# Kernel optimization log

Measured on AMD Instinct MI355X. Metric: run time of the kernel, lower is better.

Reference implementation:

```python
import jax, jax.numpy as jnp
import numpy as np

HEADS, DIM_HEADS = 16, 16
SCALE = DIM_HEADS ** -0.5

# (forward_perm, inverse_perm) for each axial dim of x: (B, S, E, H, W)
# axial axes are 1 (seq), 3 (H=4), 4 (W=5); emb axis 2 moved to last, axial axis to second-last
_PERMS = [
    ((0, 3, 4, 1, 2), (0, 3, 4, 1, 2)),  # seq axis (self-inverse)
    ((0, 1, 4, 3, 2), (0, 1, 4, 3, 2)),  # H axis (self-inverse)
    ((0, 1, 3, 4, 2), (0, 1, 4, 2, 3)),  # W axis
]


def _self_attn(x, wq, wkv, wo_w, wo_b):
    # x: (..., t, d); standard multi-head self-attention along t
    q = x @ wq.T                               # (..., t, 256)
    k, v = jnp.split(x @ wkv.T, 2, axis=-1)    # each (..., t, 256)
    lead, tlen = x.shape[:-2], x.shape[-2]
    sh = (*lead, tlen, HEADS, DIM_HEADS)
    q, k, v = q.reshape(sh), k.reshape(sh), v.reshape(sh)
    scores = jnp.einsum('...thd,...shd->...hts', q, k) * SCALE
    attn = jax.nn.softmax(scores, axis=-1)
    o = jnp.einsum('...hts,...shd->...thd', attn, v)
    o = o.reshape(*lead, tlen, HEADS * DIM_HEADS)
    return o @ wo_w.T + wo_b


def _axial_attention_layer(x, wq_l, wkv_l, wo_w_l, wo_b_l):
    # sum of attention along each axial dim (sum_axial_out=True)
    out = jnp.zeros_like(x)
    for a, (p, ip) in enumerate(_PERMS):
        y = jnp.transpose(x, p)
        y = _self_attn(y, wq_l[a], wkv_l[a], wo_w_l[a], wo_b_l[a])
        out = out + jnp.transpose(y, ip)
    return out


def setup_inputs() -> dict:
    key = jax.random.key(0)
    ks = jax.random.split(key, 8)
    B, S, E, H, W = 32, 64, 256, 4, 5
    return {
        'x': jax.random.normal(ks[0], (B, S, E, H, W), jnp.float32),
        'pos_s': jax.random.normal(ks[1], (1, S, E, 1, 1), jnp.float32),
        'pos_h': jax.random.normal(ks[2], (1, 1, E, H, 1), jnp.float32),
        'pos_w': jax.random.normal(ks[3], (1, 1, E, 1, W), jnp.float32),
        'wq': jax.random.normal(ks[4], (2, 3, 256, E), jnp.float32) * 0.02,
        'wkv': jax.random.normal(ks[5], (2, 3, 512, E), jnp.float32) * 0.02,
        'wo_w': jax.random.normal(ks[6], (2, 3, E, 256), jnp.float32) * 0.02,
        'wo_b': jnp.zeros((2, 3, E), jnp.float32),
        'dec_w': jax.random.normal(ks[7], (1, E), jnp.float32) * 0.02,
        'dec_b': jnp.zeros((1,), jnp.float32),
    }


def reference(x, pos_s, pos_h, pos_w, wq, wkv, wo_w, wo_b, dec_w, dec_b):
    # additive axial positional embeddings
    x = x + pos_s + pos_h + pos_w
    # two stacked AxialAttention blocks (no residual in the wrapper)
    for l in range(2):
        x = _axial_attention_layer(x, wq[l], wkv[l], wo_w[l], wo_b[l])
    # (B, S, E, H, W) -> (B, S, H, W, E), linear decode to 1 channel, sigmoid
    x = jnp.transpose(x, (0, 1, 3, 4, 2))
    return jax.nn.sigmoid(x @ dec_w.T + dec_b)
```

## Files before the change

kernel.cpp:

```cpp
#include <hip/hip_runtime.h>
#include <stdint.h>

typedef unsigned short u16;
typedef u16 u16x8 __attribute__((ext_vector_type(8)));
typedef __bf16 bf16x8 __attribute__((ext_vector_type(8)));
typedef float f32x4 __attribute__((ext_vector_type(4)));
typedef float f32x16 __attribute__((ext_vector_type(16)));

#define NE   256
#define NPOS 40960
#define QLD  1536

__device__ __forceinline__ float bf2f(u16 h) {
  union { unsigned u; float f; } c; c.u = ((unsigned)h) << 16; return c.f;
}
__device__ __forceinline__ u16 f2bf(float f) {
  union { float f; unsigned u; } c; c.f = f;
  unsigned u = c.u;
  return (u16)((u + 0x7FFFu + ((u >> 16) & 1u)) >> 16);
}
__device__ __forceinline__ unsigned pkbf(float a, float b) {
  unsigned r;
  asm("v_cvt_pk_bf16_f32 %0, %1, %2" : "=v"(r) : "v"(a), "v"(b));
  return r;
}
__device__ __forceinline__ void gll16(const void* g, void* l) {
  __builtin_amdgcn_global_load_lds(
      (const __attribute__((address_space(1))) void*)g,
      (__attribute__((address_space(3))) void*)l, 16, 0, 0);
}
template<int N> __device__ __forceinline__ void waitvm() {
  if constexpr (N == 0)       asm volatile("s_waitcnt vmcnt(0)"  ::: "memory");
  else if constexpr (N == 4)  asm volatile("s_waitcnt vmcnt(4)"  ::: "memory");
  else if constexpr (N == 6)  asm volatile("s_waitcnt vmcnt(6)"  ::: "memory");
  else if constexpr (N == 8)  asm volatile("s_waitcnt vmcnt(8)"  ::: "memory");
  else if constexpr (N == 12) asm volatile("s_waitcnt vmcnt(12)" ::: "memory");
}

__global__ __launch_bounds__(256) void prep_kernel(
    const float* __restrict__ x, const float* __restrict__ pos_s,
    const float* __restrict__ pos_h, const float* __restrict__ pos_w,
    u16* __restrict__ xb)
{
  __shared__ float Ls[256 * 21];
  const int bs = blockIdx.x;
  const int s  = bs & 63;
  const int tid = threadIdx.x;
  const float* xp = x + (size_t)bs * 5120;
  for (int i = tid; i < 5120; i += 256) {
    int e = i / 20, hw = i % 20;
    int h = hw / 5, w = hw % 5;
    float v = xp[i] + pos_s[s * 256 + e] + pos_h[e * 4 + h] + pos_w[e * 5 + w];
    Ls[e * 21 + hw] = v;
  }
  __syncthreads();
  u16* op = xb + (size_t)bs * 20 * 256;
  for (int i = tid; i < 5120; i += 256) {
    int nl = i >> 8, e = i & 255;
    op[nl * 256 + e] = f2bf(Ls[e * 21 + nl]);
  }
}

#define PK_T1 (6*768*256)
#define PK_T2 (2*256*768)
__global__ __launch_bounds__(256) void pack_all(
    const float* __restrict__ wq, const float* __restrict__ wkv,
    const float* __restrict__ wo, const float* __restrict__ wo_b,
    u16* __restrict__ wqp, u16* __restrict__ wop, float* __restrict__ bsum)
{
  int i = blockIdx.x * 256 + threadIdx.x;
  if (i < PK_T1) {
    int la = i / (768 * 256);
    int rem = i - la * (768 * 256);
    int r = rem >> 8, c = rem & 255;
    float v = (r < 256) ? wq[(size_t)la * 65536 + r * 256 + c] * 0.25f
                        : wkv[(size_t)la * 131072 + (r - 256) * 256 + c];
    wqp[i] = f2bf(v);
  } else if (i < PK_T1 + PK_T2) {
    int j = i - PK_T1;
    int l = j / 196608;
    int rem = j - l * 196608;
    int out = rem / 768, k = rem % 768;
    int a = k >> 8, in = k & 255;
    wop[j] = f2bf(wo[(size_t)(((l * 3 + a) * 256) + out) * 256 + in]);
  } else if (i < PK_T1 + PK_T2 + 512) {
    int j = i - PK_T1 - PK_T2;
    int l = j >> 8, c = j & 255;
    bsum[j] = wo_b[(l * 3 + 0) * 256 + c] + wo_b[(l * 3 + 1) * 256 + c]
            + wo_b[(l * 3 + 2) * 256 + c];
  }
}

template<int MODE, int NKT, int NBN>
__global__ __launch_bounds__(256, 2) void gemm_bt(
    const u16* __restrict__ A, const u16* __restrict__ B,
    u16* __restrict__ Cb, const float* __restrict__ bias,
    const float* __restrict__ dw, float* __restrict__ logit,
    int ldc)
{
  constexpr int K   = NKT * 32;
  constexpr int BN  = 128;
  constexpr int NF  = BN / 32;
  constexpr int LPT = 2 + BN / 64;
  constexpr int ASZ = 128 * 32;
  constexpr int TSZ = (128 + BN) * 32;
  static_assert(NKT >= 2, "");

  __shared__ alignas(16) u16 smem[3 * TSZ];

  const int bid = blockIdx.x;
  const int cpx = gridDim.x >> 3;
  const int mapped = (bid & 7) * cpx + (bid >> 3);
  const int bm = mapped / NBN, bn = mapped % NBN;

  const int tid  = threadIdx.x;
  const int lane = tid & 63, w = tid >> 6;
  const int wr   = (w >> 1) * 64, wc = (w & 1) * (BN / 2);
  const int r16  = lane & 15, khi = lane >> 4;

  f32x4 acc[4][NF] = {};

  const u16* gA = A + (size_t)bm * 128 * K;
  const u16* gB = B + (size_t)bn * BN * K;

  auto STAGE = [&](int kt, int which) {
    u16* As = smem + which * TSZ;
    u16* Bs = As + ASZ;
    const u16* tA = gA + kt * 32;
    const u16* tB = gB + kt * 32;
    #pragma unroll
    for (int r = 0; r < 2; ++r) {
      int i = tid + r * 256;
      int row = i >> 2, seg = (i & 3) << 3;
      gll16(tA + (size_t)row * K + seg, (char*)As + i * 16);
    }
    #pragma unroll
    for (int r = 0; r < BN / 64; ++r) {
      int i = tid + r * 256;
      int row = i >> 2, seg = (i & 3) << 3;
      gll16(tB + (size_t)row * K + seg, (char*)Bs + i * 16);
    }
  };

  STAGE(0, 0);
  STAGE(1, 1);
  #pragma unroll
  for (int kt = 0; kt < NKT; ++kt) {
    const int cur = kt % 3;
    if (kt + 2 < NKT)      { STAGE(kt + 2, (kt + 2) % 3); waitvm<2 * LPT>(); }
    else if (kt + 1 < NKT) { waitvm<LPT>(); }
    else                   { waitvm<0>(); }
    __builtin_amdgcn_s_barrier();
    asm volatile("" ::: "memory");

    const u16* As = smem + cur * TSZ;
    const u16* Bs = As + ASZ;
    bf16x8 af[4], bfr[NF];
    #pragma unroll
    for (int m = 0; m < 4; ++m)
      af[m] = *(const bf16x8*)(As + (wr + m * 16 + r16) * 32 + khi * 8);
    #pragma unroll
    for (int n = 0; n < NF; ++n)
      bfr[n] = *(const bf16x8*)(Bs + (wc + n * 16 + r16) * 32 + khi * 8);
    #pragma unroll
    for (int m = 0; m < 4; ++m)
      #pragma unroll
      for (int n = 0; n < NF; ++n)
        acc[m][n] = __builtin_amdgcn_mfma_f32_16x16x32_bf16(af[m], bfr[n], acc[m][n], 0, 0, 0);

    asm volatile("" ::: "memory");
    __builtin_amdgcn_s_barrier();
  }

  const int row0 = bm * 128 + wr + khi * 4;
  const int col0 = bn * BN + wc + r16;

  if constexpr (MODE == 4) {
    float dwv[NF], bvv[NF];
    #pragma unroll
    for (int n = 0; n < NF; ++n) {
      int c = col0 + n * 16;
      dwv[n] = dw[c];
      bvv[n] = bias[c];
    }
    #pragma unroll
    for (int m = 0; m < 4; ++m) {
      #pragma unroll
      for (int j = 0; j < 4; ++j) {
        float p = 0.f;
        #pragma unroll
        for (int n = 0; n < NF; ++n) p += (acc[m][n][j] + bvv[n]) * dwv[n];
        p += __shfl_xor(p, 1);
        p += __shfl_xor(p, 2);
        p += __shfl_xor(p, 4);
        p += __shfl_xor(p, 8);
        if (r16 == 0) atomicAdd(&logit[row0 + m * 16 + j], p);
      }
    }
  } else {
    #pragma unroll
    for (int m = 0; m < 4; ++m) {
      #pragma unroll
      for (int n = 0; n < NF; ++n) {
        int c = col0 + n * 16;
        float bv = (MODE == 3) ? bias[c] : 0.f;
        #pragma unroll
        for (int j = 0; j < 4; ++j) {
          int r = row0 + m * 16 + j;
          Cb[(size_t)r * ldc + c] = f2bf(acc[m][n][j] + bv);
        }
      }
    }
  }
}

__global__ __launch_bounds__(256) void attn_seq_mfma(
    const u16* __restrict__ QKV, u16* __restrict__ Ob)
{
  const int w = threadIdx.x >> 6, lane = threadIdx.x & 63;
  const int wid = blockIdx.x * 4 + w;
  const int hd = wid & 15, g = wid >> 4;
  const int gb = g / 20, gr = g % 20;
  const int nbase = gb * 1280 + gr;
  const int lo = lane & 31, hi = lane >> 5;

  bf16x8 kf[2], qf[2];
  #pragma unroll
  for (int t = 0; t < 2; ++t) {
    size_t r = (size_t)(nbase + (lo + 32 * t) * 20) * QLD;
    kf[t] = *(const bf16x8*)(QKV + r + 256 + hd * 16 + hi * 8);
    qf[t] = *(const bf16x8*)(QKV + r +       hd * 16 + hi * 8);
  }
  union { u16 a[8]; bf16x8 v; } vt[4];
  #pragma unroll
  for (int c = 0; c < 4; ++c)
    #pragma unroll
    for (int j = 0; j < 8; ++j)
      vt[c].a[j] = QKV[(size_t)(nbase + (c * 16 + hi * 8 + j) * 20) * QLD
                       + 512 + hd * 16 + lo];

  f32x16 s00 = {}, s10 = {}, s01 = {}, s11 = {};
  s00 = __builtin_amdgcn_mfma_f32_32x32x16_bf16(kf[0], qf[0], s00, 0, 0, 0);
  s10 = __builtin_amdgcn_mfma_f32_32x32x16_bf16(kf[1], qf[0], s10, 0, 0, 0);
  s01 = __builtin_amdgcn_mfma_f32_32x32x16_bf16(kf[0], qf[1], s01, 0, 0, 0);
  s11 = __builtin_amdgcn_mfma_f32_32x32x16_bf16(kf[1], qf[1], s11, 0, 0, 0);

  auto run_qt = [&](f32x16 t0, f32x16 t1, int qt) {
    float m = -1e30f;
    #pragma unroll
    for (int r = 0; r < 16; ++r) { m = fmaxf(m, t0[r]); m = fmaxf(m, t1[r]); }
    m = fmaxf(m, __shfl_xor(m, 32));
    const float C = 1.4426950408889634f;
    float mc = m * C;
    float sum = 0.f;
    #pragma unroll
    for (int r = 0; r < 16; ++r) {
      float p0 = __builtin_amdgcn_exp2f(t0[r] * C - mc);
      float p1 = __builtin_amdgcn_exp2f(t1[r] * C - mc);
      t0[r] = p0; t1[r] = p1; sum += p0; sum += p1;
    }
    sum += __shfl_xor(sum, 32);
    float inv = __builtin_amdgcn_rcpf(sum);
    #pragma unroll
    for (int r = 0; r < 16; ++r) { t0[r] *= inv; t1[r] *= inv; }

    f32x16 oa = {};
    #pragma unroll
    for (int c = 0; c < 4; ++c) {
      const int rb = 8 * (c & 1);
      const f32x16& tt = (c < 2) ? t0 : t1;
      unsigned X0 = pkbf(tt[rb + 0], tt[rb + 1]);
      unsigned X1 = pkbf(tt[rb + 2], tt[rb + 3]);
      unsigned Y0 = pkbf(tt[rb + 4], tt[rb + 5]);
      unsigned Y1 = pkbf(tt[rb + 6], tt[rb + 7]);
      unsigned X0p = __shfl_xor((int)X0, 32), X1p = __shfl_xor((int)X1, 32);
      unsigned Y0p = __shfl_xor((int)Y0, 32), Y1p = __shfl_xor((int)Y1, 32);
      union { unsigned u[4]; bf16x8 v; } pf;
      pf.u[0] = hi ? Y0p : X0;
      pf.u[1] = hi ? Y1p : X1;
      pf.u[2] = hi ? Y0  : X0p;
      pf.u[3] = hi ? Y1  : X1p;
      oa = __builtin_amdgcn_mfma_f32_32x32x16_bf16(vt[c].v, pf.v, oa, 0, 0, 0);
    }
    unsigned P0 = pkbf(oa[0], oa[1]);
    unsigned P1 = pkbf(oa[2], oa[3]);
    unsigned P2 = pkbf(oa[4], oa[5]);
    unsigned P3 = pkbf(oa[6], oa[7]);
    unsigned sP0 = __shfl_xor((int)P0, 32), sP1 = __shfl_xor((int)P1, 32);
    unsigned sP2 = __shfl_xor((int)P2, 32), sP3 = __shfl_xor((int)P3, 32);
    union { unsigned u[4]; u16x8 v; } ov;
    ov.u[0] = hi ? sP2 : P0;
    ov.u[1] = hi ? sP3 : P1;
    ov.u[2] = hi ? P2  : sP0;
    ov.u[3] = hi ? P3  : sP1;
    u16* po = Ob + (size_t)(nbase + (qt * 32 + lo) * 20) * 768 + hd * 16 + hi * 8;
    *(u16x8*)po = ov.v;
  };
  run_qt(s00, s10, 0);
  run_qt(s01, s11, 1);
}

template<int T>
__device__ __forceinline__ void attn1(
    const u16* __restrict__ QKV, int n, int base, int stp, int hd,
    u16* __restrict__ po)
{
  const u16* qp = QKV + (size_t)n * QLD + hd * 16;
  u16x8 q0 = *(const u16x8*)(qp), q1 = *(const u16x8*)(qp + 8);
  float q[16];
  #pragma unroll
  for (int d = 0; d < 8; ++d) { q[d] = bf2f(q0[d]); q[d + 8] = bf2f(q1[d]); }

  float s[T];
  float m = -1e30f;
  #pragma unroll
  for (int j = 0; j < T; ++j) {
    const u16* kp = QKV + (size_t)(base + j * stp) * QLD + 256 + hd * 16;
    u16x8 k0 = *(const u16x8*)(kp), k1 = *(const u16x8*)(kp + 8);
    float a = 0.f;
    #pragma unroll
    for (int d = 0; d < 8; ++d) a += q[d] * bf2f(k0[d]) + q[d + 8] * bf2f(k1[d]);
    s[j] = a;
    m = fmaxf(m, a);
  }
  float sum = 0.f;
  float o[16];
  #pragma unroll
  for (int d = 0; d < 16; ++d) o[d] = 0.f;
  #pragma unroll
  for (int j = 0; j < T; ++j) {
    float pj = __expf(s[j] - m);
    sum += pj;
    const u16* vp = QKV + (size_t)(base + j * stp) * QLD + 512 + hd * 16;
    u16x8 w0 = *(const u16x8*)(vp), w1 = *(const u16x8*)(vp + 8);
    #pragma unroll
    for (int d = 0; d < 8; ++d) { o[d] += pj * bf2f(w0[d]); o[d + 8] += pj * bf2f(w1[d]); }
  }
  float inv = 1.0f / sum;
  u16x8 r0, r1;
  #pragma unroll
  for (int d = 0; d < 8; ++d) { r0[d] = f2bf(o[d] * inv); r1[d] = f2bf(o[d + 8] * inv); }
  *(u16x8*)(po)     = r0;
  *(u16x8*)(po + 8) = r1;
}

__global__ __launch_bounds__(256) void attn_hw(
    const u16* __restrict__ QKV, u16* __restrict__ Ob)
{
  const int tg = blockIdx.x * 256 + threadIdx.x;
  const int hd = tg & 15, n = tg >> 4;
  int h  = (n % 20) / 5;
  int w5 = n % 5;
  attn1<4>(QKV,       n, n - h * 5, 5, hd, Ob + (size_t)n * 768 + 256 + hd * 16);
  attn1<5>(QKV + 768, n, n - w5,    1, hd, Ob + (size_t)n * 768 + 512 + hd * 16);
}

__global__ __launch_bounds__(256) void sigmoid_kernel(
    const float* __restrict__ logit, const float* __restrict__ dec_b,
    float* __restrict__ out)
{
  int i = blockIdx.x * 256 + threadIdx.x;
  out[i] = 1.0f / (1.0f + __expf(-(logit[i] + dec_b[0])));
}

extern "C" void kernel_launch(void* const* d_in, const int* in_sizes, int n_in,
                              void* d_out, int out_size, void* d_ws, size_t ws_size,
                              hipStream_t stream) {
  const float* x     = (const float*)d_in[0];
  const float* pos_s = (const float*)d_in[1];
  const float* pos_h = (const float*)d_in[2];
  const float* pos_w = (const float*)d_in[3];
  const float* wq    = (const float*)d_in[4];
  const float* wkv   = (const float*)d_in[5];
  const float* wo_w  = (const float*)d_in[6];
  const float* wo_b  = (const float*)d_in[7];
  const float* dec_w = (const float*)d_in[8];
  const float* dec_b = (const float*)d_in[9];
  float* out = (float*)d_out;

  char* ws = (char*)d_ws;
  u16*   xb    = (u16*)ws;
  u16*   Ob    = (u16*)(ws + 20971520);
  u16*   QKV   = (u16*)(ws + 83886080);
  u16*   wqp   = (u16*)(ws + 209715200);
  u16*   wop   = (u16*)(ws + 212074496);
  float* bsum  = (float*)(ws + 212860928);
  float* logit = (float*)(ws + 212862976);

  prep_kernel<<<2048, 256, 0, stream>>>(x, pos_s, pos_h, pos_w, xb);
  pack_all<<<(PK_T1 + PK_T2 + 512 + 255) / 256, 256, 0, stream>>>(
      wq, wkv, wo_w, wo_b, wqp, wop, bsum);
  hipMemsetAsync(logit, 0, NPOS * sizeof(float), stream);

  for (int l = 0; l < 2; ++l) {
    gemm_bt<0, 8, 6><<<320 * 6, 256, 0, stream>>>(
        xb, wqp + (size_t)(l * 3) * 196608, QKV, nullptr, nullptr, nullptr, QLD);
    attn_seq_mfma<<<2560, 256, 0, stream>>>(QKV, Ob);
    gemm_bt<0, 8, 12><<<320 * 12, 256, 0, stream>>>(
        xb, wqp + (size_t)(l * 3 + 1) * 196608, QKV, nullptr, nullptr, nullptr, QLD);
    attn_hw<<<2560, 256, 0, stream>>>(QKV, Ob);
    if (l == 0)
      gemm_bt<3, 24, 2><<<320 * 2, 256, 0, stream>>>(
          Ob, wop, xb, bsum, nullptr, nullptr, 256);
    else
      gemm_bt<4, 24, 2><<<320 * 2, 256, 0, stream>>>(
          Ob, wop + 196608, nullptr, bsum + 256, dec_w, logit, 0);
  }

  sigmoid_kernel<<<NPOS / 256, 256, 0, stream>>>(logit, dec_b, out);
}
```

Measured before the change: 345.1 us.

## Fuse H/W axis QKV projection and attention into one LDS-resident kernel

Replaces the separate QKV GEMM for the H and W axes, plus the global-memory attention kernel, with one kernel. Each 320-thread block computes QKV for 80 positions with MFMA into shared memory, then runs the short 4- and 5-length attentions directly from LDS. This removes the global write and reread of a large QKV buffer and one launch, and halves the QKV workspace stride. In exchange the B-operand weights are read straight from global memory with no LDS tiling, and blocks use about 124KB of LDS, which limits occupancy.

```diff
diff --git a/kernel.cpp b/kernel.cpp
--- a/kernel.cpp
+++ b/kernel.cpp
@@ -9,7 +9,7 @@
 
 #define NE   256
 #define NPOS 40960
-#define QLD  1536
+#define QLD  768
 
 __device__ __forceinline__ float bf2f(u16 h) {
   union { unsigned u; float f; } c; c.u = ((unsigned)h) << 16; return c.f;
@@ -300,59 +300,110 @@
   run_qt(s01, s11, 1);
 }
 
-template<int T>
-__device__ __forceinline__ void attn1(
-    const u16* __restrict__ QKV, int n, int base, int stp, int hd,
-    u16* __restrict__ po)
-{
-  const u16* qp = QKV + (size_t)n * QLD + hd * 16;
-  u16x8 q0 = *(const u16x8*)(qp), q1 = *(const u16x8*)(qp + 8);
-  float q[16];
+__global__ __launch_bounds__(320) void fused_hw(
+    const u16* __restrict__ xb, const u16* __restrict__ wqp_l,
+    u16* __restrict__ Ob)
+{
+  __shared__ u16 qkv[80][776];
+  const int tid = threadIdx.x;
+  const int w = tid >> 6, lane = tid & 63;
+  const int n0 = blockIdx.x * 80;
+  const int r16 = lane & 15, khi = lane >> 4;
+  const int arow = n0 + w * 16 + r16;
+
+  bf16x8 af[8];
   #pragma unroll
-  for (int d = 0; d < 8; ++d) { q[d] = bf2f(q0[d]); q[d + 8] = bf2f(q1[d]); }
-
-  float s[T];
-  float m = -1e30f;
+  for (int ks = 0; ks < 8; ++ks)
+    af[ks] = *(const bf16x8*)(xb + (size_t)arow * 256 + ks * 32 + khi * 8);
+
   #pragma unroll
-  for (int j = 0; j < T; ++j) {
-    const u16* kp = QKV + (size_t)(base + j * stp) * QLD + 256 + hd * 16;
-    u16x8 k0 = *(const u16x8*)(kp), k1 = *(const u16x8*)(kp + 8);
-    float a = 0.f;
-    #pragma unroll
-    for (int d = 0; d < 8; ++d) a += q[d] * bf2f(k0[d]) + q[d + 8] * bf2f(k1[d]);
-    s[j] = a;
-    m = fmaxf(m, a);
-  }
-  float sum = 0.f;
-  float o[16];
-  #pragma unroll
-  for (int d = 0; d < 16; ++d) o[d] = 0.f;
-  #pragma unroll
-  for (int j = 0; j < T; ++j) {
-    float pj = __expf(s[j] - m);
-    sum += pj;
-    const u16* vp = QKV + (size_t)(base + j * stp) * QLD + 512 + hd * 16;
-    u16x8 w0 = *(const u16x8*)(vp), w1 = *(const u16x8*)(vp + 8);
-    #pragma unroll
-    for (int d = 0; d < 8; ++d) { o[d] += pj * bf2f(w0[d]); o[d + 8] += pj * bf2f(w1[d]); }
-  }
-  float inv = 1.0f / sum;
-  u16x8 r0, r1;
-  #pragma unroll
-  for (int d = 0; d < 8; ++d) { r0[d] = f2bf(o[d] * inv); r1[d] = f2bf(o[d + 8] * inv); }
-  *(u16x8*)(po)     = r0;
-  *(u16x8*)(po + 8) = r1;
-}
-
-__global__ __launch_bounds__(256) void attn_hw(
-    const u16* __restrict__ QKV, u16* __restrict__ Ob)
-{
-  const int tg = blockIdx.x * 256 + threadIdx.x;
-  const int hd = tg & 15, n = tg >> 4;
-  int h  = (n % 20) / 5;
-  int w5 = n % 5;
-  attn1<4>(QKV,       n, n - h * 5, 5, hd, Ob + (size_t)n * 768 + 256 + hd * 16);
-  attn1<5>(QKV + 768, n, n - w5,    1, hd, Ob + (size_t)n * 768 + 512 + hd * 16);
+  for (int axis = 0; axis < 2; ++axis) {
+    const u16* wb = wqp_l + (size_t)axis * 196608;
+    if (axis) __syncthreads();
+
+    for (int hd = 0; hd < 16; ++hd) {
+      f32x4 acc[3] = {};
+      #pragma unroll
+      for (int nf = 0; nf < 3; ++nf) {
+        const u16* wrow = wb + (size_t)(nf * 256 + hd * 16 + r16) * 256;
+        #pragma unroll
+        for (int ks = 0; ks < 8; ++ks) {
+          bf16x8 bf = *(const bf16x8*)(wrow + ks * 32 + khi * 8);
+          acc[nf] = __builtin_amdgcn_mfma_f32_16x16x32_bf16(af[ks], bf, acc[nf], 0, 0, 0);
+        }
+      }
+      #pragma unroll
+      for (int nf = 0; nf < 3; ++nf)
+        #pragma unroll
+        for (int j = 0; j < 4; ++j)
+          qkv[w * 16 + khi * 4 + j][nf * 256 + hd * 16 + r16] = f2bf(acc[nf][j]);
+    }
+    __syncthreads();
+
+    const int T = axis ? 5 : 4;
+    const int ng = axis ? 16 : 20;
+    if (tid < ng * 16) {
+      const int g = tid >> 4, hd = tid & 15;
+      int rbase, rstp;
+      if (axis == 0) { rbase = (g / 5) * 20 + (g % 5);     rstp = 5; }
+      else           { rbase = (g / 4) * 20 + (g % 4) * 5; rstp = 1; }
+      float kk[5][16];
+      #pragma unroll
+      for (int j = 0; j < 5; ++j) {
+        if (j < T) {
+          const u16* kp = &qkv[rbase + j * rstp][256 + hd * 16];
+          u16x8 a0 = *(const u16x8*)kp, a1 = *(const u16x8*)(kp + 8);
+          #pragma unroll
+          for (int d = 0; d < 8; ++d) {
+            kk[j][d] = bf2f(a0[d]); kk[j][d + 8] = bf2f(a1[d]);
+          }
+        }
+      }
+      for (int i = 0; i < T; ++i) {
+        const int r = rbase + i * rstp;
+        const u16* qp = &qkv[r][hd * 16];
+        u16x8 q0 = *(const u16x8*)qp, q1 = *(const u16x8*)(qp + 8);
+        float q[16];
+        #pragma unroll
+        for (int d = 0; d < 8; ++d) { q[d] = bf2f(q0[d]); q[d + 8] = bf2f(q1[d]); }
+        float s[5], m = -1e30f;
+        #pragma unroll
+        for (int j = 0; j < 5; ++j) {
+          if (j < T) {
+            float a = 0.f;
+            #pragma unroll
+            for (int d = 0; d < 16; ++d) a += q[d] * kk[j][d];
+            s[j] = a; m = fmaxf(m, a);
+          }
+        }
+        float sum = 0.f, o[16];
+        #pragma unroll
+        for (int d = 0; d < 16; ++d) o[d] = 0.f;
+        #pragma unroll
+        for (int j = 0; j < 5; ++j) {
+          if (j < T) {
+            float pj = __expf(s[j] - m);
+            sum += pj;
+            const u16* vp = &qkv[rbase + j * rstp][512 + hd * 16];
+            u16x8 v0 = *(const u16x8*)vp, v1 = *(const u16x8*)(vp + 8);
+            #pragma unroll
+            for (int d = 0; d < 8; ++d) {
+              o[d] += pj * bf2f(v0[d]); o[d + 8] += pj * bf2f(v1[d]);
+            }
+          }
+        }
+        float inv = 1.0f / sum;
+        u16x8 r0, r1;
+        #pragma unroll
+        for (int d = 0; d < 8; ++d) {
+          r0[d] = f2bf(o[d] * inv); r1[d] = f2bf(o[d + 8] * inv);
+        }
+        u16* po = Ob + (size_t)(n0 + r) * 768 + 256 + axis * 256 + hd * 16;
+        *(u16x8*)(po)     = r0;
+        *(u16x8*)(po + 8) = r1;
+      }
+    }
+  }
 }
 
 __global__ __launch_bounds__(256) void sigmoid_kernel(
@@ -382,10 +433,10 @@
   u16*   xb    = (u16*)ws;
   u16*   Ob    = (u16*)(ws + 20971520);
   u16*   QKV   = (u16*)(ws + 83886080);
-  u16*   wqp   = (u16*)(ws + 209715200);
-  u16*   wop   = (u16*)(ws + 212074496);
-  float* bsum  = (float*)(ws + 212860928);
-  float* logit = (float*)(ws + 212862976);
+  u16*   wqp   = (u16*)(ws + 146800640);
+  u16*   wop   = (u16*)(ws + 149159936);
+  float* bsum  = (float*)(ws + 149946368);
+  float* logit = (float*)(ws + 149948416);
 
   prep_kernel<<<2048, 256, 0, stream>>>(x, pos_s, pos_h, pos_w, xb);
   pack_all<<<(PK_T1 + PK_T2 + 512 + 255) / 256, 256, 0, stream>>>(
@@ -396,9 +447,8 @@
     gemm_bt<0, 8, 6><<<320 * 6, 256, 0, stream>>>(
         xb, wqp + (size_t)(l * 3) * 196608, QKV, nullptr, nullptr, nullptr, QLD);
     attn_seq_mfma<<<2560, 256, 0, stream>>>(QKV, Ob);
-    gemm_bt<0, 8, 12><<<320 * 12, 256, 0, stream>>>(
-        xb, wqp + (size_t)(l * 3 + 1) * 196608, QKV, nullptr, nullptr, nullptr, QLD);
-    attn_hw<<<2560, 256, 0, stream>>>(QKV, Ob);
+    fused_hw<<<NPOS / 80, 320, 0, stream>>>(
+        xb, wqp + (size_t)(l * 3 + 1) * 196608, Ob);
     if (l == 0)
       gemm_bt<3, 24, 2><<<320 * 2, 256, 0, stream>>>(
           Ob, wop, xb, bsum, nullptr, nullptr, 256);
```

Result: slower. 638.9 us (+85.2%).

## Add B-resident streaming GEMM for QKV projections processing multiple M tiles per block

Applied to the files above, without the earlier changes.

Adds a new gemm_stream kernel that loads the whole 128xK weight tile into LDS once and then walks four consecutive 128-row A tiles, double-buffering A k-slices with global_load_lds. It replaces the MODE 0 QKV projection GEMMs, so the grids become 480 and 960 blocks instead of 1920 and 3840. The aim is to stop reloading the weight tile for every output tile and to spread launch and prologue costs over more work. In exchange there are fewer blocks, more LDS per block, and a barrier on every k-step with only two A buffers to overlap loads.

```diff
diff --git a/kernel.cpp b/kernel.cpp
--- a/kernel.cpp
+++ b/kernel.cpp
@@ -31,6 +31,7 @@
 }
 template<int N> __device__ __forceinline__ void waitvm() {
   if constexpr (N == 0)       asm volatile("s_waitcnt vmcnt(0)"  ::: "memory");
+  else if constexpr (N == 2)  asm volatile("s_waitcnt vmcnt(2)"  ::: "memory");
   else if constexpr (N == 4)  asm volatile("s_waitcnt vmcnt(4)"  ::: "memory");
   else if constexpr (N == 6)  asm volatile("s_waitcnt vmcnt(6)"  ::: "memory");
   else if constexpr (N == 8)  asm volatile("s_waitcnt vmcnt(8)"  ::: "memory");
@@ -91,6 +92,92 @@
   }
 }
 
+template<int NKT, int NBN, int TPB>
+__global__ __launch_bounds__(256, 2) void gemm_stream(
+    const u16* __restrict__ A, const u16* __restrict__ B,
+    u16* __restrict__ Cb, int ldc)
+{
+  constexpr int K     = NKT * 32;
+  constexpr int NSTEP = NKT * TPB;
+  __shared__ alignas(16) u16 Bs[128 * K];
+  __shared__ alignas(16) u16 As[2][128 * 32];
+
+  const int nblk = gridDim.x;
+  const int bid  = blockIdx.x;
+  const int mapped = (bid & 7) * (nblk >> 3) + (bid >> 3);
+  const int strip = mapped / NBN, bn = mapped % NBN;
+  const int bm0 = strip * TPB;
+
+  const int tid  = threadIdx.x;
+  const int lane = tid & 63, w = tid >> 6;
+  const int wr   = (w >> 1) * 64, wc = (w & 1) * 64;
+  const int r16  = lane & 15, khi = lane >> 4;
+
+  const u16* gB = B + (size_t)bn * 128 * K;
+  const u16* gA = A + (size_t)bm0 * 128 * K;
+
+  #pragma unroll
+  for (int b = 0; b < K / 16; ++b) {
+    int slot = tid + b * 256;
+    int kt = slot >> 9, rem = slot & 511;
+    int row = rem >> 2, c = rem & 3;
+    gll16(gB + (size_t)row * K + kt * 32 + c * 8, (char*)Bs + slot * 16);
+  }
+
+  auto STAGE_A = [&](int g) {
+    const int t = g / NKT, kt = g % NKT;
+    const u16* tA = gA + (size_t)t * 128 * K + kt * 32;
+    u16* dst = As[g & 1];
+    #pragma unroll
+    for (int r = 0; r < 2; ++r) {
+      int i = tid + r * 256;
+      int row = i >> 2, seg = (i & 3) << 3;
+      gll16(tA + (size_t)row * K + seg, (char*)dst + i * 16);
+    }
+  };
+
+  f32x4 acc[4][4] = {};
+  STAGE_A(0);
+
+  for (int t = 0; t < TPB; ++t) {
+    #pragma unroll
+    for (int kt = 0; kt < NKT; ++kt) {
+      const int g = t * NKT + kt;
+      __builtin_amdgcn_s_barrier();
+      if (g + 1 < NSTEP) { STAGE_A(g + 1); waitvm<2>(); }
+      else               { waitvm<0>(); }
+      asm volatile("" ::: "memory");
+
+      const u16* Ab = As[g & 1];
+      const u16* Bk = Bs + kt * (128 * 32);
+      bf16x8 af[4], bfr[4];
+      #pragma unroll
+      for (int m = 0; m < 4; ++m)
+        af[m] = *(const bf16x8*)(Ab + (wr + m * 16 + r16) * 32 + khi * 8);
+      #pragma unroll
+      for (int n = 0; n < 4; ++n)
+        bfr[n] = *(const bf16x8*)(Bk + (wc + n * 16 + r16) * 32 + khi * 8);
+      #pragma unroll
+      for (int m = 0; m < 4; ++m)
+        #pragma unroll
+        for (int n = 0; n < 4; ++n)
+          acc[m][n] = __builtin_amdgcn_mfma_f32_16x16x32_bf16(af[m], bfr[n], acc[m][n], 0, 0, 0);
+      asm volatile("" ::: "memory");
+    }
+    const int row0 = (bm0 + t) * 128 + wr + khi * 4;
+    const int col0 = bn * 128 + wc + r16;
+    #pragma unroll
+    for (int m = 0; m < 4; ++m)
+      #pragma unroll
+      for (int n = 0; n < 4; ++n)
+        #pragma unroll
+        for (int j = 0; j < 4; ++j) {
+          Cb[(size_t)(row0 + m * 16 + j) * ldc + col0 + n * 16] = f2bf(acc[m][n][j]);
+          acc[m][n][j] = 0.f;
+        }
+  }
+}
+
 template<int MODE, int NKT, int NBN>
 __global__ __launch_bounds__(256, 2) void gemm_bt(
     const u16* __restrict__ A, const u16* __restrict__ B,
@@ -393,11 +480,11 @@
   hipMemsetAsync(logit, 0, NPOS * sizeof(float), stream);
 
   for (int l = 0; l < 2; ++l) {
-    gemm_bt<0, 8, 6><<<320 * 6, 256, 0, stream>>>(
-        xb, wqp + (size_t)(l * 3) * 196608, QKV, nullptr, nullptr, nullptr, QLD);
+    gemm_stream<8, 6, 4><<<480, 256, 0, stream>>>(
+        xb, wqp + (size_t)(l * 3) * 196608, QKV, QLD);
     attn_seq_mfma<<<2560, 256, 0, stream>>>(QKV, Ob);
-    gemm_bt<0, 8, 12><<<320 * 12, 256, 0, stream>>>(
-        xb, wqp + (size_t)(l * 3 + 1) * 196608, QKV, nullptr, nullptr, nullptr, QLD);
+    gemm_stream<8, 12, 4><<<960, 256, 0, stream>>>(
+        xb, wqp + (size_t)(l * 3 + 1) * 196608, QKV, QLD);
     attn_hw<<<2560, 256, 0, stream>>>(QKV, Ob);
     if (l == 0)
       gemm_bt<3, 24, 2><<<320 * 2, 256, 0, stream>>>(
```

Result: faster. 335.2 us (-2.8%).
